# Kernel tuning notes

Hardware: AMD Instinct MI355X
Metric: run time of the kernel (lower is better)

The kernel has to match this reference:

```python
import jax, jax.numpy as jnp
import numpy as np

K_PERIODS = 6


def setup_inputs() -> dict:
    key = jax.random.key(0)
    x = jax.random.normal(key, (16, 2048, 128), dtype=jnp.float32)
    return {"x": x}


def reference(x):
    # x: [B, T, N] -> out: [B, K, Pmax, N].
    # Pmax is data-dependent in the torch original (max selected period); here we
    # use the static upper bound Pmax = T so shapes are jit-static. Columns
    # p >= P_row are zero, matching the original's zero padding.
    B, T, N = x.shape
    BN = B * N
    seqs = jnp.transpose(x, (0, 2, 1)).reshape(BN, T)  # [BN, T]

    # --- top-k nonzero frequencies by spectral energy ---
    spec = jnp.fft.rfft(seqs, axis=-1)
    mag2 = spec.real ** 2 + spec.imag ** 2
    mag2 = mag2.at[:, 0].set(0.0)  # kill DC bin
    k = min(K_PERIODS, mag2.shape[-1] - 1)
    _, kidx = jax.lax.top_k(mag2, k)          # [BN, K]
    kidx = jnp.maximum(kidx, 1)

    # --- per-(row, freq) period geometry ---
    P = jnp.maximum(T // kidx, 1)             # [BN, K] period length
    cycles = jnp.maximum(T // P, 1)           # [BN, K] number of full cycles
    take = cycles * P
    base = jnp.maximum(T - take, 0)           # [BN, K] start offset

    # --- fold-and-average via scatter-add (no [BN,K,Cmax,Pmax] blowup) ---
    # element at time t >= base maps to phase p = (t - base) % P, averaged over cycles
    t = jnp.arange(T, dtype=jnp.int32)
    rel = t[None, None, :] - base[:, :, None]          # [BN, K, T]
    valid = rel >= 0
    p = jnp.where(valid, rel % P[:, :, None], 0)       # phase index in [0, P)
    vals = jnp.where(valid, seqs[:, None, :], 0.0)     # [BN, K, T]

    row = jnp.arange(BN * k, dtype=jnp.int32).reshape(BN, k, 1)
    seg_ids = row * T + p                               # flat segment id
    sums = jax.ops.segment_sum(vals.reshape(-1), seg_ids.reshape(-1),
                               num_segments=BN * k * T)
    seg = sums.reshape(BN, k, T) / cycles[:, :, None].astype(vals.dtype)

    out = seg.reshape(B, N, k, T).transpose(0, 2, 3, 1)  # [B, K, Pmax=T, N]
    return out
```

## Files before the change

kernel.cpp:

```cpp
#include <hip/hip_runtime.h>
#include <stdint.h>

#define TB   256
#define TLEN 2048
#define NB   16
#define NCH  128
#define BN   (NB*NCH)
#define KP   6

typedef unsigned long long u64;

__device__ inline float2 cmul(float2 a, float2 b) {
  return make_float2(a.x * b.x - a.y * b.y, a.x * b.y + a.y * b.x);
}

__global__ __launch_bounds__(256) void k_fill0(float4* __restrict__ out, int n4) {
  int i = blockIdx.x * blockDim.x + threadIdx.x;
  int stride = gridDim.x * blockDim.x;
  float4 z = make_float4(0.f, 0.f, 0.f, 0.f);
  for (; i < n4; i += stride) out[i] = z;
}

__global__ __launch_bounds__(256) void k_transpose_in(const float* __restrict__ x,
                                                      float* __restrict__ seqs) {
  __shared__ float tile[64][65];
  int t0 = blockIdx.x * 64, n0 = blockIdx.y * 64, b = blockIdx.z;
  int tx = threadIdx.x & 63, ty = threadIdx.x >> 6;
#pragma unroll
  for (int tt = ty; tt < 64; tt += 4)
    tile[tt][tx] = x[(size_t)(b * TLEN + t0 + tt) * NCH + n0 + tx];
  __syncthreads();
#pragma unroll
  for (int nn = ty; nn < 64; nn += 4)
    seqs[(size_t)(b * NCH + n0 + nn) * TLEN + t0 + tx] = tile[tx][nn];
}

#define PAD(o) ((o) + ((o) >> 4))
__global__ __launch_bounds__(256) void k_fft_topk(const float* __restrict__ seqs,
                                                  int4* __restrict__ params) {
  __shared__ float2 bufA[2176];
  __shared__ float2 bufB[2176];
  __shared__ float2 tw[512];
  __shared__ u64 wmax[4];
  int tid = threadIdx.x;
  int lane = tid & 63, wv = tid >> 6;
  int r0 = blockIdx.x * 2;

  for (int t = tid; t < TLEN; t += TB) {
    float vr = seqs[(size_t)r0 * TLEN + t];
    float vi = seqs[(size_t)(r0 + 1) * TLEN + t];
    bufA[PAD(t)] = make_float2(vr, vi);
  }
  const float c0 = -6.283185307179586f / 2048.0f;
  for (int j = tid; j < 512; j += TB) {
    float sn, cs;
    sincosf(c0 * (float)j, &sn, &cs);
    tw[j] = make_float2(cs, sn);
  }

  float2* xb = bufA;
  float2* yb = bufB;
#pragma unroll 1
  for (int st2 = 0; st2 < 10; st2 += 2) {
    int s = 1 << st2;
    __syncthreads();
#pragma unroll
    for (int ii = 0; ii < 2; ii++) {
      int i = tid + ii * TB;
      int q = i & (s - 1);
      int cb = i - q;
      float2 A0 = xb[PAD(i)];
      float2 A1 = xb[PAD(i + 512)];
      float2 A2 = xb[PAD(i + 1024)];
      float2 A3 = xb[PAD(i + 1536)];
      float2 S02 = make_float2(A0.x + A2.x, A0.y + A2.y);
      float2 D02 = make_float2(A0.x - A2.x, A0.y - A2.y);
      float2 S13 = make_float2(A1.x + A3.x, A1.y + A3.y);
      float2 D13 = make_float2(A1.x - A3.x, A1.y - A3.y);
      float2 b0 = make_float2(S02.x + S13.x, S02.y + S13.y);
      float2 b1 = make_float2(D02.x + D13.y, D02.y - D13.x);
      float2 b2 = make_float2(S02.x - S13.x, S02.y - S13.y);
      float2 b3 = make_float2(D02.x - D13.y, D02.y + D13.x);
      float2 w1 = tw[cb];
      float2 w2 = make_float2(w1.x * w1.x - w1.y * w1.y, 2.f * w1.x * w1.y);
      float2 w3 = cmul(w1, w2);
      int o = q + 4 * cb;
      yb[PAD(o)]         = b0;
      yb[PAD(o + s)]     = cmul(w1, b1);
      yb[PAD(o + 2 * s)] = cmul(w2, b2);
      yb[PAD(o + 3 * s)] = cmul(w3, b3);
    }
    float2* t2 = xb; xb = yb; yb = t2;
  }
  __syncthreads();
#pragma unroll
  for (int ii = 0; ii < 4; ii++) {
    int i = tid + ii * TB;
    float2 a = xb[PAD(i)];
    float2 b = xb[PAD(i + 1024)];
    yb[PAD(i)]        = make_float2(a.x + b.x, a.y + b.y);
    yb[PAD(i + 1024)] = make_float2(a.x - b.x, a.y - b.y);
  }
  __syncthreads();
  const float2* Z = bufA;
  u64* keys = (u64*)bufB;
  for (int i = tid; i < 1024; i += TB) {
    int kb = i + 1;
    float2 zk = Z[PAD(kb)];
    float2 zc = Z[PAD(2048 - kb)];
    float ax = zk.x + zc.x, ay = zk.y - zc.y;
    float bx = zk.x - zc.x, by = zk.y + zc.y;
    float m2a = ax * ax + ay * ay;
    float m2b = bx * bx + by * by;
    keys[i]        = ((u64)__float_as_uint(m2a) << 32) | (unsigned)(0xFFFFFFFFu - (unsigned)kb);
    keys[1024 + i] = ((u64)__float_as_uint(m2b) << 32) | (unsigned)(0xFFFFFFFFu - (unsigned)kb);
  }
  __syncthreads();

  int rw = wv >> 1;
  u64* kb2 = keys + rw * 1024;
  int t2 = tid & 127;
  for (int r = 0; r < KP; r++) {
    u64 best = 0ull;
    for (int i = t2; i < 1024; i += 128) {
      u64 v = kb2[i];
      best = v > best ? v : best;
    }
    for (int off = 32; off > 0; off >>= 1) {
      u64 o = __shfl_down(best, off);
      best = o > best ? o : best;
    }
    if (lane == 0) wmax[wv] = best;
    __syncthreads();
    if ((tid & 127) == 0) {
      u64 b0 = wmax[rw * 2], b1 = wmax[rw * 2 + 1];
      best = b0 > b1 ? b0 : b1;
      int bin = (int)(0xFFFFFFFFu - (unsigned)(best & 0xFFFFFFFFull));
      if (bin < 1 || bin > 1024) bin = 1;
      kb2[bin - 1] = 0ull;
      int P = TLEN / bin;
      int cyc = TLEN / P;
      int base = TLEN - cyc * P;
      params[(r0 + rw) * KP + r] = make_int4(P, base, cyc, 0);
    }
    __syncthreads();
  }
}

__global__ __launch_bounds__(256) void k_fold_row(const float* __restrict__ seqs,
                                                  const int4* __restrict__ params,
                                                  float* __restrict__ out) {
  __shared__ float srow[TLEN];
  int row = blockIdx.x;
  int b = row >> 7, n = row & 127;
  int tid = threadIdx.x, lane = tid & 63, wv = tid >> 6;

  const float4* s4 = (const float4*)(seqs + (size_t)row * TLEN);
  float4* r4 = (float4*)srow;
  for (int i = tid; i < TLEN / 4; i += TB) r4[i] = s4[i];
  __syncthreads();

  for (int k = wv; k < KP; k += 4) {
    int4 pr = params[row * KP + k];
    int P = pr.x, base = pr.y, cyc = pr.z;
    float inv = 1.0f / (float)cyc;
    float* dst = out + (size_t)(b * KP + k) * TLEN * NCH + n;

    if (P >= 64) {
      for (int p = lane; p < P; p += 64) {
        const float* sp = srow + base + p;
        float s = 0.f;
        for (int c = 0; c < cyc; c++) s += sp[c * P];
        dst[(size_t)p * NCH] = s * inv;
      }
    } else {
      int wc = 64 / P;
      int u = wc * P;
      int ci = lane / P;
      float v = 0.f;
      if (lane < u) {
        for (int c0 = 0; c0 < cyc; c0 += wc) {
          int c = c0 + ci;
          if (c < cyc) v += srow[base + c0 * P + lane];
        }
      }
      for (int s = P; s < u; s <<= 1) {
        float o = __shfl_down(v, s);
        if (lane + s < u) v += o;
      }
      if (lane < P) dst[(size_t)lane * NCH] = v * inv;
    }
  }
}

extern "C" void kernel_launch(void* const* d_in, const int* in_sizes, int n_in,
                              void* d_out, int out_size, void* d_ws, size_t ws_size,
                              hipStream_t stream) {
  const float* x = (const float*)d_in[0];
  float* out = (float*)d_out;
  char* ws = (char*)d_ws;

  const size_t seqs_bytes = (size_t)BN * TLEN * 4;
  float* seqs = (float*)ws;
  int4* params = (int4*)(ws + seqs_bytes);

  k_fill0<<<8192, 256, 0, stream>>>((float4*)out, out_size / 4);
  k_transpose_in<<<dim3(TLEN / 64, NCH / 64, NB), 256, 0, stream>>>(x, seqs);
  k_fft_topk<<<dim3(BN / 2), 256, 0, stream>>>(seqs, params);
  k_fold_row<<<dim3(BN), 256, 0, stream>>>(seqs, params, out);
}
```

Baseline: 154.3 us.

## Fuse fill/transpose, switch FFT to radix-8, and merge fold into FFT kernel

Merges the zero-fill and the input transpose into one launch. Replaces the radix-4 FFT stages with three radix-8 stages plus a final radix-4 stage, so there are fewer shared-memory passes and barriers. Folds the period-averaging step into the FFT/top-k kernel, keeping the selected parameters in shared memory so the separate fold kernel and its launch go away. The cost is a heavier register load per thread and a fold phase that now runs on only 1024 blocks.

```diff
diff --git a/kernel.cpp b/kernel.cpp
--- a/kernel.cpp
+++ b/kernel.cpp
@@ -13,95 +13,119 @@
 __device__ inline float2 cmul(float2 a, float2 b) {
   return make_float2(a.x * b.x - a.y * b.y, a.x * b.y + a.y * b.x);
 }
-
-__global__ __launch_bounds__(256) void k_fill0(float4* __restrict__ out, int n4) {
-  int i = blockIdx.x * blockDim.x + threadIdx.x;
-  int stride = gridDim.x * blockDim.x;
-  float4 z = make_float4(0.f, 0.f, 0.f, 0.f);
-  for (; i < n4; i += stride) out[i] = z;
-}
-
-__global__ __launch_bounds__(256) void k_transpose_in(const float* __restrict__ x,
-                                                      float* __restrict__ seqs) {
-  __shared__ float tile[64][65];
-  int t0 = blockIdx.x * 64, n0 = blockIdx.y * 64, b = blockIdx.z;
-  int tx = threadIdx.x & 63, ty = threadIdx.x >> 6;
-#pragma unroll
-  for (int tt = ty; tt < 64; tt += 4)
-    tile[tt][tx] = x[(size_t)(b * TLEN + t0 + tt) * NCH + n0 + tx];
-  __syncthreads();
-#pragma unroll
-  for (int nn = ty; nn < 64; nn += 4)
-    seqs[(size_t)(b * NCH + n0 + nn) * TLEN + t0 + tx] = tile[tx][nn];
+__device__ inline float2 cadd(float2 a, float2 b) { return make_float2(a.x + b.x, a.y + b.y); }
+__device__ inline float2 csub(float2 a, float2 b) { return make_float2(a.x - b.x, a.y - b.y); }
+__device__ inline float2 cmni(float2 a) { return make_float2(a.y, -a.x); }
+
+__global__ __launch_bounds__(256) void k_prep(const float* __restrict__ x,
+                                              float* __restrict__ seqs,
+                                              float4* __restrict__ out4, int n4) {
+  int bid = blockIdx.x;
+  if (bid < 1024) {
+    __shared__ float tile[64][65];
+    int tb = bid & 31, nb = (bid >> 5) & 1, b = bid >> 6;
+    int t0 = tb * 64, n0 = nb * 64;
+    int tx = threadIdx.x & 63, ty = threadIdx.x >> 6;
+#pragma unroll
+    for (int tt = ty; tt < 64; tt += 4)
+      tile[tt][tx] = x[(size_t)(b * TLEN + t0 + tt) * NCH + n0 + tx];
+    __syncthreads();
+#pragma unroll
+    for (int nn = ty; nn < 64; nn += 4)
+      seqs[(size_t)(b * NCH + n0 + nn) * TLEN + t0 + tx] = tile[tx][nn];
+  } else {
+    int i = (bid - 1024) * 256 + threadIdx.x;
+    if (i < n4) out4[i] = make_float4(0.f, 0.f, 0.f, 0.f);
+  }
 }
 
 #define PAD(o) ((o) + ((o) >> 4))
-__global__ __launch_bounds__(256) void k_fft_topk(const float* __restrict__ seqs,
-                                                  int4* __restrict__ params) {
-  __shared__ float2 bufA[2176];
-  __shared__ float2 bufB[2176];
-  __shared__ float2 tw[512];
+#define C2 0.70710678118654752f
+
+__global__ __launch_bounds__(256) void k_fft_fold(const float* __restrict__ seqs,
+                                                  float* __restrict__ out) {
+  __shared__ __align__(16) float2 bufA[2176];
+  __shared__ __align__(16) float2 bufB[2176];
+  __shared__ float2 tw[256];
   __shared__ u64 wmax[4];
-  int tid = threadIdx.x;
-  int lane = tid & 63, wv = tid >> 6;
+  __shared__ int4 prm[2][KP];
+  int tid = threadIdx.x, lane = tid & 63, wv = tid >> 6;
   int r0 = blockIdx.x * 2;
-
-  for (int t = tid; t < TLEN; t += TB) {
-    float vr = seqs[(size_t)r0 * TLEN + t];
-    float vi = seqs[(size_t)(r0 + 1) * TLEN + t];
-    bufA[PAD(t)] = make_float2(vr, vi);
-  }
-  const float c0 = -6.283185307179586f / 2048.0f;
-  for (int j = tid; j < 512; j += TB) {
+  const float* row0 = seqs + (size_t)r0 * TLEN;
+
+#pragma unroll
+  for (int k = 0; k < 8; k++) {
+    int t = tid + k * TB;
+    bufA[PAD(t)] = make_float2(row0[t], row0[t + TLEN]);
+  }
+  {
     float sn, cs;
-    sincosf(c0 * (float)j, &sn, &cs);
-    tw[j] = make_float2(cs, sn);
+    sincosf((-6.283185307179586f / 2048.f) * (float)tid, &sn, &cs);
+    tw[tid & 255] = make_float2(cs, sn);
   }
 
   float2* xb = bufA;
   float2* yb = bufB;
-#pragma unroll 1
-  for (int st2 = 0; st2 < 10; st2 += 2) {
-    int s = 1 << st2;
-    __syncthreads();
-#pragma unroll
-    for (int ii = 0; ii < 2; ii++) {
-      int i = tid + ii * TB;
-      int q = i & (s - 1);
-      int cb = i - q;
-      float2 A0 = xb[PAD(i)];
-      float2 A1 = xb[PAD(i + 512)];
-      float2 A2 = xb[PAD(i + 1024)];
-      float2 A3 = xb[PAD(i + 1536)];
-      float2 S02 = make_float2(A0.x + A2.x, A0.y + A2.y);
-      float2 D02 = make_float2(A0.x - A2.x, A0.y - A2.y);
-      float2 S13 = make_float2(A1.x + A3.x, A1.y + A3.y);
-      float2 D13 = make_float2(A1.x - A3.x, A1.y - A3.y);
-      float2 b0 = make_float2(S02.x + S13.x, S02.y + S13.y);
-      float2 b1 = make_float2(D02.x + D13.y, D02.y - D13.x);
-      float2 b2 = make_float2(S02.x - S13.x, S02.y - S13.y);
-      float2 b3 = make_float2(D02.x - D13.y, D02.y + D13.x);
-      float2 w1 = tw[cb];
-      float2 w2 = make_float2(w1.x * w1.x - w1.y * w1.y, 2.f * w1.x * w1.y);
-      float2 w3 = cmul(w1, w2);
-      int o = q + 4 * cb;
-      yb[PAD(o)]         = b0;
-      yb[PAD(o + s)]     = cmul(w1, b1);
-      yb[PAD(o + 2 * s)] = cmul(w2, b2);
-      yb[PAD(o + 3 * s)] = cmul(w3, b3);
-    }
-    float2* t2 = xb; xb = yb; yb = t2;
+#pragma unroll
+  for (int stage = 0; stage < 3; stage++) {
+    int s = (stage == 0) ? 1 : (stage == 1) ? 8 : 64;
+    __syncthreads();
+    int i = tid;
+    int q = i & (s - 1);
+    int cb = i - q;
+    float2 A0 = xb[PAD(i)],        A1 = xb[PAD(i + 256)],
+           A2 = xb[PAD(i + 512)],  A3 = xb[PAD(i + 768)],
+           A4 = xb[PAD(i + 1024)], A5 = xb[PAD(i + 1280)],
+           A6 = xb[PAD(i + 1536)], A7 = xb[PAD(i + 1792)];
+    float2 s02 = cadd(A0, A4), d02 = csub(A0, A4);
+    float2 s13 = cadd(A2, A6), d13 = csub(A2, A6);
+    float2 E0 = cadd(s02, s13), E1 = cadd(d02, cmni(d13));
+    float2 E2 = csub(s02, s13), E3 = csub(d02, cmni(d13));
+    float2 t02 = cadd(A1, A5), e02 = csub(A1, A5);
+    float2 t13 = cadd(A3, A7), e13 = csub(A3, A7);
+    float2 O0 = cadd(t02, t13), O1 = cadd(e02, cmni(e13));
+    float2 O2 = csub(t02, t13), O3 = csub(e02, cmni(e13));
+    float2 T0 = O0;
+    float2 T1 = make_float2(C2 * (O1.x + O1.y), C2 * (O1.y - O1.x));
+    float2 T2 = cmni(O2);
+    float2 T3 = make_float2(C2 * (O3.y - O3.x), -C2 * (O3.x + O3.y));
+    float2 B0 = cadd(E0, T0), B4 = csub(E0, T0);
+    float2 B1 = cadd(E1, T1), B5 = csub(E1, T1);
+    float2 B2 = cadd(E2, T2), B6 = csub(E2, T2);
+    float2 B3 = cadd(E3, T3), B7 = csub(E3, T3);
+    float2 w1 = tw[cb];
+    float2 w2 = cmul(w1, w1);
+    float2 w3 = cmul(w2, w1);
+    float2 w4 = cmul(w2, w2);
+    float2 w5 = cmul(w4, w1);
+    float2 w6 = cmul(w4, w2);
+    float2 w7 = cmul(w4, w3);
+    int o = q + 8 * cb;
+    yb[PAD(o)]         = B0;
+    yb[PAD(o + s)]     = cmul(w1, B1);
+    yb[PAD(o + 2 * s)] = cmul(w2, B2);
+    yb[PAD(o + 3 * s)] = cmul(w3, B3);
+    yb[PAD(o + 4 * s)] = cmul(w4, B4);
+    yb[PAD(o + 5 * s)] = cmul(w5, B5);
+    yb[PAD(o + 6 * s)] = cmul(w6, B6);
+    yb[PAD(o + 7 * s)] = cmul(w7, B7);
+    float2* tp = xb; xb = yb; yb = tp;
   }
   __syncthreads();
 #pragma unroll
-  for (int ii = 0; ii < 4; ii++) {
+  for (int ii = 0; ii < 2; ii++) {
     int i = tid + ii * TB;
-    float2 a = xb[PAD(i)];
-    float2 b = xb[PAD(i + 1024)];
-    yb[PAD(i)]        = make_float2(a.x + b.x, a.y + b.y);
-    yb[PAD(i + 1024)] = make_float2(a.x - b.x, a.y - b.y);
+    float2 a0 = xb[PAD(i)], a1 = xb[PAD(i + 512)];
+    float2 a2 = xb[PAD(i + 1024)], a3 = xb[PAD(i + 1536)];
+    float2 S02 = cadd(a0, a2), D02 = csub(a0, a2);
+    float2 S13 = cadd(a1, a3), D13 = csub(a1, a3);
+    yb[PAD(i)]        = cadd(S02, S13);
+    yb[PAD(i + 512)]  = cadd(D02, cmni(D13));
+    yb[PAD(i + 1024)] = csub(S02, S13);
+    yb[PAD(i + 1536)] = csub(D02, cmni(D13));
   }
   __syncthreads();
+
   const float2* Z = bufA;
   u64* keys = (u64*)bufB;
   for (int i = tid; i < 1024; i += TB) {
@@ -117,8 +141,15 @@
   }
   __syncthreads();
 
-  int rw = wv >> 1;
-  u64* kb2 = keys + rw * 1024;
+  float* srows = (float*)bufA;
+  {
+    const float4* s4 = (const float4*)row0;
+    float4* r4 = (float4*)srows;
+    for (int i = tid; i < 1024; i += TB) r4[i] = s4[i];
+  }
+
+  int rw2 = wv >> 1;
+  u64* kb2 = keys + rw2 * 1024;
   int t2 = tid & 127;
   for (int r = 0; r < KP; r++) {
     u64 best = 0ull;
@@ -132,8 +163,8 @@
     }
     if (lane == 0) wmax[wv] = best;
     __syncthreads();
-    if ((tid & 127) == 0) {
-      u64 b0 = wmax[rw * 2], b1 = wmax[rw * 2 + 1];
+    if (t2 == 0) {
+      u64 b0 = wmax[rw2 * 2], b1 = wmax[rw2 * 2 + 1];
       best = b0 > b1 ? b0 : b1;
       int bin = (int)(0xFFFFFFFFu - (unsigned)(best & 0xFFFFFFFFull));
       if (bin < 1 || bin > 1024) bin = 1;
@@ -141,29 +172,18 @@
       int P = TLEN / bin;
       int cyc = TLEN / P;
       int base = TLEN - cyc * P;
-      params[(r0 + rw) * KP + r] = make_int4(P, base, cyc, 0);
-    }
-    __syncthreads();
-  }
-}
-
-__global__ __launch_bounds__(256) void k_fold_row(const float* __restrict__ seqs,
-                                                  const int4* __restrict__ params,
-                                                  float* __restrict__ out) {
-  __shared__ float srow[TLEN];
-  int row = blockIdx.x;
-  int b = row >> 7, n = row & 127;
-  int tid = threadIdx.x, lane = tid & 63, wv = tid >> 6;
-
-  const float4* s4 = (const float4*)(seqs + (size_t)row * TLEN);
-  float4* r4 = (float4*)srow;
-  for (int i = tid; i < TLEN / 4; i += TB) r4[i] = s4[i];
-  __syncthreads();
-
-  for (int k = wv; k < KP; k += 4) {
-    int4 pr = params[row * KP + k];
+      prm[rw2][r] = make_int4(P, base, cyc, 0);
+    }
+    __syncthreads();
+  }
+
+  for (int task = wv; task < 2 * KP; task += 4) {
+    int rw = task & 1, k = task >> 1;
+    int4 pr = prm[rw][k];
     int P = pr.x, base = pr.y, cyc = pr.z;
     float inv = 1.0f / (float)cyc;
+    const float* srow = srows + rw * TLEN;
+    int row = r0 + rw, b = row >> 7, n = row & 127;
     float* dst = out + (size_t)(b * KP + k) * TLEN * NCH + n;
 
     if (P >= 64) {
@@ -174,9 +194,7 @@
         dst[(size_t)p * NCH] = s * inv;
       }
     } else {
-      int wc = 64 / P;
-      int u = wc * P;
-      int ci = lane / P;
+      int wc = 64 / P, u = wc * P, ci = lane / P;
       float v = 0.f;
       if (lane < u) {
         for (int c0 = 0; c0 < cyc; c0 += wc) {
@@ -198,14 +216,10 @@
                               hipStream_t stream) {
   const float* x = (const float*)d_in[0];
   float* out = (float*)d_out;
-  char* ws = (char*)d_ws;
-
-  const size_t seqs_bytes = (size_t)BN * TLEN * 4;
-  float* seqs = (float*)ws;
-  int4* params = (int4*)(ws + seqs_bytes);
-
-  k_fill0<<<8192, 256, 0, stream>>>((float4*)out, out_size / 4);
-  k_transpose_in<<<dim3(TLEN / 64, NCH / 64, NB), 256, 0, stream>>>(x, seqs);
-  k_fft_topk<<<dim3(BN / 2), 256, 0, stream>>>(seqs, params);
-  k_fold_row<<<dim3(BN), 256, 0, stream>>>(seqs, params, out);
-}
+  float* seqs = (float*)d_ws;
+
+  int n4 = out_size / 4;
+  int fill_blocks = (n4 + 255) / 256;
+  k_prep<<<1024 + fill_blocks, 256, 0, stream>>>(x, seqs, (float4*)out, n4);
+  k_fft_fold<<<BN / 2, 256, 0, stream>>>(seqs, out);
+}
```

New measurement: 145.1 us. 6.0% less time.
